# Optimization experiments

Hardware: AMD Instinct MI355X
Metric: run time of the kernel (lower is better)

## Reference

```python
import jax, jax.numpy as jnp
import numpy as np

B, C, H, W = 8, 256, 64, 64
CK = C // 8  # query/key channels


def setup_inputs() -> dict:
    key = jax.random.key(0)
    ks = jax.random.split(key, 8)
    s = 1.0 / np.sqrt(C)
    return {
        "x": jax.random.normal(ks[0], (B, C, H, W), dtype=jnp.float32),
        "Wq": jax.random.normal(ks[1], (CK, C), dtype=jnp.float32) * s,
        "bq": jax.random.normal(ks[2], (CK,), dtype=jnp.float32) * 0.01,
        "Wk": jax.random.normal(ks[3], (CK, C), dtype=jnp.float32) * s,
        "bk": jax.random.normal(ks[4], (CK,), dtype=jnp.float32) * 0.01,
        "Wv": jax.random.normal(ks[5], (C, C), dtype=jnp.float32) * s,
        "bv": jax.random.normal(ks[6], (C,), dtype=jnp.float32) * 0.01,
        "gamma": jax.random.normal(ks[7], (1,), dtype=jnp.float32) * 0.1,
    }


def reference(x, Wq, bq, Wk, bk, Wv, bv, gamma):
    b, c, h, w = x.shape
    n = h * w
    xf = x.reshape(b, c, n)                       # [B,C,N]
    # 1x1 convs == channel-wise linear maps
    q = jnp.einsum('oc,bcn->bon', Wq, xf) + bq[:, None]   # [B,CK,N]
    k = jnp.einsum('oc,bcn->bon', Wk, xf) + bk[:, None]   # [B,CK,N]
    v = jnp.einsum('oc,bcn->bon', Wv, xf) + bv[:, None]   # [B,C,N]
    energy = jnp.einsum('bcm,bcn->bmn', q, k)             # [B,N,N] (query rows m)
    attn = jax.nn.softmax(energy, axis=-1)
    out = jnp.einsum('bcn,bmn->bcm', v, attn)             # value @ attn^T
    out = out.reshape(b, c, h, w)
    return gamma * out + x
```

## Files before the change

kernel.cpp:

```cpp
#include <hip/hip_runtime.h>
#include <stdint.h>

typedef unsigned short u16;
typedef unsigned int u32;
typedef __bf16 bf16_t;
typedef __bf16 bf16x4 __attribute__((ext_vector_type(4)));
typedef __bf16 bf16x8 __attribute__((ext_vector_type(8)));
typedef float f32x4 __attribute__((ext_vector_type(4)));
typedef float f32x16 __attribute__((ext_vector_type(16)));

#define LOG2E 1.4426950408889634f
#define MFMA32(a, b, c) __builtin_amdgcn_mfma_f32_32x32x16_bf16(a, b, c, 0, 0, 0)

__device__ __forceinline__ u16 f2bf(float f) {
    union { float f; unsigned int u; } v; v.f = f;
    unsigned int r = v.u + 0x7fffu + ((v.u >> 16) & 1u);
    return (u16)(r >> 16);
}

__device__ __forceinline__ bf16x8 ld8f_bf(const float* __restrict__ p) {
    float4 a = *reinterpret_cast<const float4*>(p);
    float4 b = *reinterpret_cast<const float4*>(p + 4);
    bf16x8 r;
    r[0] = (bf16_t)a.x; r[1] = (bf16_t)a.y; r[2] = (bf16_t)a.z; r[3] = (bf16_t)a.w;
    r[4] = (bf16_t)b.x; r[5] = (bf16_t)b.y; r[6] = (bf16_t)b.z; r[7] = (bf16_t)b.w;
    return r;
}

__device__ __forceinline__ u32 cvt_pk_bf16(float a, float b) {
    u32 r;
    asm("v_cvt_pk_bf16_f32 %0, %1, %2" : "=v"(r) : "v"(a), "v"(b));
    return r;
}

__device__ __forceinline__ void plane32_swap(u32& a, u32& b) {
    asm("v_permlane32_swap_b32 %0, %1" : "+v"(a), "+v"(b));
}

__device__ __forceinline__ bf16x8 pack8(const float* p) {
    u32 c0 = cvt_pk_bf16(p[0], p[1]);
    u32 c1 = cvt_pk_bf16(p[2], p[3]);
    u32 c2 = cvt_pk_bf16(p[4], p[5]);
    u32 c3 = cvt_pk_bf16(p[6], p[7]);
    plane32_swap(c0, c2);
    plane32_swap(c1, c3);
    union { u32 u[4]; bf16x8 v; } f;
    f.u[0] = c0; f.u[1] = c1; f.u[2] = c2; f.u[3] = c3;
    return f.v;
}

__device__ __forceinline__ void g2lds16(const u16* g, u16* l) {
    __builtin_amdgcn_global_load_lds(
        (const __attribute__((address_space(1))) unsigned int*)g,
        (__attribute__((address_space(3))) unsigned int*)l, 16, 0, 0);
}

__global__ __launch_bounds__(256) void k_transpose(
    const float* __restrict__ x,
    const float* __restrict__ Wq, const float* __restrict__ Wk,
    const float* __restrict__ Wv,
    u16* __restrict__ xT, u16* __restrict__ wqkb, u16* __restrict__ wvb) {
    int blk = blockIdx.x;
    int t = threadIdx.x;
    if (blk >= 2048) {
        if (blk == 2048) {
            for (int j = 0; j < 8; ++j) {
                int fg = j * 256 + t;
                int n = fg >> 5, g = fg & 31;
                const float* src = (n < 32) ? (Wq + (size_t)n * 256 + g * 8)
                                            : (Wk + (size_t)(n - 32) * 256 + g * 8);
                *reinterpret_cast<bf16x8*>(wqkb + n * 256 + ((g ^ (n & 7)) << 3)) =
                    ld8f_bf(src);
            }
        } else {
            int base = (blk - 2049) * 2048;
            for (int j = 0; j < 8; ++j) {
                int fg = base + j * 256 + t;
                int slice = fg >> 10, d = fg & 1023;
                int co = d >> 2, g2 = (d & 3) ^ (co & 3);
                *reinterpret_cast<bf16x8*>(wvb + fg * 8) =
                    ld8f_bf(Wv + (size_t)co * 256 + slice * 32 + g2 * 8);
            }
        }
        return;
    }
    __shared__ u16 tile[64][68];
    int b = blk >> 8;
    int r = blk & 255;
    int c0 = (r & 3) * 64;
    int n0 = (r >> 2) * 64;
    const float* xb = x + (size_t)b * 256 * 4096;
    u16* xTb = xT + (size_t)b * 4096 * 256;
    int lc = t >> 4;
    int l4 = (t & 15) * 4;
    #pragma unroll
    for (int p = 0; p < 4; ++p) {
        int c = lc + p * 16;
        float4 v = *reinterpret_cast<const float4*>(xb + (size_t)(c0 + c) * 4096 + n0 + l4);
        tile[c][l4 + 0] = f2bf(v.x); tile[c][l4 + 1] = f2bf(v.y);
        tile[c][l4 + 2] = f2bf(v.z); tile[c][l4 + 3] = f2bf(v.w);
    }
    __syncthreads();
    #pragma unroll
    for (int p = 0; p < 4; ++p) {
        int n = lc + p * 16;
        ushort4 v;
        v.x = tile[l4 + 0][n]; v.y = tile[l4 + 1][n];
        v.z = tile[l4 + 2][n]; v.w = tile[l4 + 3][n];
        int gslot = ((c0 + l4) >> 3) ^ ((n0 + n) & 7);
        *reinterpret_cast<ushort4*>(
            xTb + (size_t)(n0 + n) * 256 + (gslot << 3) + (l4 & 7)) = v;
    }
}

__global__ __launch_bounds__(256, 2) void k_proj(
    const u16* __restrict__ xT, const u16* __restrict__ wqkb,
    const u16* __restrict__ wvb,
    const float* __restrict__ bq, const float* __restrict__ bk,
    const float* __restrict__ bv,
    u16* __restrict__ qt, u16* __restrict__ kt, u16* __restrict__ vt) {
    __shared__ u16 Xs[64 * 256];
    __shared__ u16 Ws[64 * 256];
    __shared__ u16 Wvs[256 * 32];
    int blk = blockIdx.x;
    int b = blk & 7;
    int n0 = (blk >> 3) * 64;
    int t = threadIdx.x;
    int w = t >> 6;
    int lane = t & 63;
    int lo = lane & 15;
    int q = lane >> 4;
    const u16* xTb = xT + (size_t)b * 4096 * 256;

    #pragma unroll
    for (int p = 0; p < 8; ++p) {
        g2lds16(xTb + (size_t)n0 * 256 + (p * 256 + t) * 8, &Xs[(p * 256 + w * 64) * 8]);
        g2lds16(wqkb + (p * 256 + t) * 8, &Ws[(p * 256 + w * 64) * 8]);
    }

    f32x4 accqk[4] = {};
    f32x4 accv[16];
    #pragma unroll
    for (int i = 0; i < 16; ++i) accv[i] = f32x4{0.f, 0.f, 0.f, 0.f};

    int rowA = w * 16 + lo;
    int cw = w * 64;
    for (int c0 = 0; c0 < 256; c0 += 32) {
        __syncthreads();
        #pragma unroll
        for (int p = 0; p < 4; ++p) {
            g2lds16(wvb + (size_t)(c0 >> 5) * 8192 + (p * 256 + t) * 8,
                    &Wvs[(p * 256 + w * 64) * 8]);
        }
        __syncthreads();

        int K = c0 >> 3;
        bf16x8 a = *reinterpret_cast<const bf16x8*>(
            &Xs[(rowA * 32 + ((K + q) ^ (lo & 7))) * 8]);
        #pragma unroll
        for (int ot = 0; ot < 4; ++ot) {
            bf16x8 bb = *reinterpret_cast<const bf16x8*>(
                &Ws[((ot * 16 + lo) * 32 + ((K + q) ^ (lo & 7))) * 8]);
            accqk[ot] = __builtin_amdgcn_mfma_f32_16x16x32_bf16(a, bb, accqk[ot], 0, 0, 0);
        }
        bf16x8 xbf[4];
        #pragma unroll
        for (int nt = 0; nt < 4; ++nt)
            xbf[nt] = *reinterpret_cast<const bf16x8*>(
                &Xs[((nt * 16 + lo) * 32 + ((K + q) ^ (lo & 7))) * 8]);
        #pragma unroll
        for (int ct = 0; ct < 4; ++ct) {
            int co = cw + ct * 16 + lo;
            bf16x8 av = *reinterpret_cast<const bf16x8*>(
                &Wvs[(co * 4 + (q ^ (co & 3))) * 8]);
            #pragma unroll
            for (int nt = 0; nt < 4; ++nt)
                accv[ct * 4 + nt] = __builtin_amdgcn_mfma_f32_16x16x32_bf16(
                    av, xbf[nt], accv[ct * 4 + nt], 0, 0, 0);
        }
    }
    #pragma unroll
    for (int ot = 0; ot < 4; ++ot) {
        float bias = (ot < 2) ? bq[ot * 16 + lo] : bk[(ot - 2) * 16 + lo];
        #pragma unroll
        for (int r = 0; r < 4; ++r) {
            int n = n0 + w * 16 + q * 4 + r;
            float val = accqk[ot][r] + bias;
            if (ot < 2) qt[((size_t)b * 4096 + n) * 32 + ot * 16 + lo] = f2bf(val * LOG2E);
            else        kt[((size_t)b * 4096 + n) * 32 + (ot - 2) * 16 + lo] = f2bf(val);
        }
    }
    #pragma unroll
    for (int ct = 0; ct < 4; ++ct) {
        #pragma unroll
        for (int nt = 0; nt < 4; ++nt) {
            int nt_g = (n0 >> 4) + nt;
            #pragma unroll
            for (int r = 0; r < 4; ++r) {
                int co = cw + ct * 16 + q * 4 + r;
                float val = accv[ct * 4 + nt][r] + bv[co];
                vt[(((size_t)b * 256 + nt_g) * 256 + co) * 16 + lo] = f2bf(val);
            }
        }
    }
}

#define FLASH_PV_HALF1(FC0, FC1, Vc_)                                          \
    {                                                                          \
        bf16x8 v0_ = *reinterpret_cast<const bf16x8*>(Vc_ + gslot8);           \
        bf16x8 v1_ = *reinterpret_cast<const bf16x8*>(Vc_ + 512 + gslot8);     \
        bf16x8 v2_ = *reinterpret_cast<const bf16x8*>(Vc_ + 1024 + gslot8);    \
        bf16x8 v3_ = *reinterpret_cast<const bf16x8*>(Vc_ + 1536 + gslot8);    \
        O0 = MFMA32(v0_, FC0, O0); O1 = MFMA32(v1_, FC0, O1);                  \
        O2 = MFMA32(v2_, FC0, O2); O3 = MFMA32(v3_, FC0, O3);                  \
        bf16x8 v4_ = *reinterpret_cast<const bf16x8*>(Vc_ + 2048 + gslot8);    \
        bf16x8 v5_ = *reinterpret_cast<const bf16x8*>(Vc_ + 2560 + gslot8);    \
        bf16x8 v6_ = *reinterpret_cast<const bf16x8*>(Vc_ + 3072 + gslot8);    \
        bf16x8 v7_ = *reinterpret_cast<const bf16x8*>(Vc_ + 3584 + gslot8);    \
        O0 = MFMA32(v4_, FC1, O0); O1 = MFMA32(v5_, FC1, O1);                  \
        O2 = MFMA32(v6_, FC1, O2); O3 = MFMA32(v7_, FC1, O3);                  \
    }

#define FLASH_PV_HALF2(FC2, FC3, Vc_)                                          \
    {                                                                          \
        bf16x8 v0_ = *reinterpret_cast<const bf16x8*>(Vc_ + 4096 + gslot8);    \
        bf16x8 v1_ = *reinterpret_cast<const bf16x8*>(Vc_ + 4608 + gslot8);    \
        bf16x8 v2_ = *reinterpret_cast<const bf16x8*>(Vc_ + 5120 + gslot8);    \
        bf16x8 v3_ = *reinterpret_cast<const bf16x8*>(Vc_ + 5632 + gslot8);    \
        O0 = MFMA32(v0_, FC2, O0); O1 = MFMA32(v1_, FC2, O1);                  \
        O2 = MFMA32(v2_, FC2, O2); O3 = MFMA32(v3_, FC2, O3);                  \
        bf16x8 v4_ = *reinterpret_cast<const bf16x8*>(Vc_ + 6144 + gslot8);    \
        bf16x8 v5_ = *reinterpret_cast<const bf16x8*>(Vc_ + 6656 + gslot8);    \
        bf16x8 v6_ = *reinterpret_cast<const bf16x8*>(Vc_ + 7168 + gslot8);    \
        bf16x8 v7_ = *reinterpret_cast<const bf16x8*>(Vc_ + 7680 + gslot8);    \
        O0 = MFMA32(v4_, FC3, O0); O1 = MFMA32(v5_, FC3, O1);                  \
        O2 = MFMA32(v6_, FC3, O2); O3 = MFMA32(v7_, FC3, O3);                  \
    }

#define FLASH_ITER(S_, KC0, KC1, KC2, KC3, KN0, KN1, KN2, KN3,                 \
                   FC0, FC1, FC2, FC3, FN0, FN1, FN2, FN3, VDN)                \
    {                                                                          \
        const int s_ = (S_);                                                   \
        const u16* kp_ = kbase + (size_t)(((s_ + 2) & 63) * 2048);             \
        KN0 = *reinterpret_cast<const bf16x8*>(kp_);                           \
        KN1 = *reinterpret_cast<const bf16x8*>(kp_ + 16);                      \
        KN2 = *reinterpret_cast<const bf16x8*>(kp_ + 1024);                    \
        KN3 = *reinterpret_cast<const bf16x8*>(kp_ + 1040);                    \
        const u16* vs_ = vstage + (size_t)(s_ + 1) * 16384;                    \
        g2lds16(vs_,        VDN);                                              \
        g2lds16(vs_ + 512,  VDN + 512);                                        \
        g2lds16(vs_ + 1024, VDN + 1024);                                       \
        g2lds16(vs_ + 1536, VDN + 1536);                                       \
        f32x16 S0_ = MFMA32(KC0, qf0, z16); S0_ = MFMA32(KC1, qf1, S0_);       \
        f32x16 S1_ = MFMA32(KC2, qf0, z16); S1_ = MFMA32(KC3, qf1, S1_);       \
        const u16* Vc_ = Vs[s_ & 1];                                           \
        float p0_[16];                                                         \
        _Pragma("unroll")                                                      \
        for (int i_ = 0; i_ < 16; ++i_) {                                      \
            p0_[i_] = __builtin_amdgcn_exp2f(S0_[i_]); lsum += p0_[i_];        \
        }                                                                      \
        FN0 = pack8(p0_); FN1 = pack8(p0_ + 8);                                \
        FLASH_PV_HALF1(FC0, FC1, Vc_)                                          \
        float p1_[16];                                                         \
        _Pragma("unroll")                                                      \
        for (int i_ = 0; i_ < 16; ++i_) {                                      \
            p1_[i_] = __builtin_amdgcn_exp2f(S1_[i_]); lsum += p1_[i_];        \
        }                                                                      \
        FN2 = pack8(p1_); FN3 = pack8(p1_ + 8);                                \
        FLASH_PV_HALF2(FC2, FC3, Vc_)                                          \
        __syncthreads();                                                       \
    }

__global__ __launch_bounds__(256, 2) void k_flash(
    const u16* __restrict__ qt, const u16* __restrict__ kt,
    const u16* __restrict__ vt, const float* __restrict__ x,
    const float* __restrict__ gamma, float* __restrict__ out) {
    __shared__ u16 Vs[2][8192];
    int blk = blockIdx.x;
    int b = blk & 7;
    int rest = blk >> 3;
    int m0 = (rest & 31) * 128;
    int ch0 = (rest >> 5) * 128;
    int t = threadIdx.x;
    int w = t >> 6;
    int lane = t & 63;
    int la = lane & 31;
    int hi = lane >> 5;

    const u16* qtb = qt + (size_t)b * 4096 * 32;
    const u16* ktb = kt + (size_t)b * 4096 * 32;
    const u16* vtb = vt + (size_t)b * 256 * 256 * 16;

    int qw0 = m0 + w * 32;
    bf16x8 qf0 = *reinterpret_cast<const bf16x8*>(qtb + (size_t)(qw0 + la) * 32 + hi * 8);
    bf16x8 qf1 = *reinterpret_cast<const bf16x8*>(qtb + (size_t)(qw0 + la) * 32 + 16 + hi * 8);

    const u16* kbase = ktb + (size_t)la * 32 + hi * 8;

    int g = la * 2 + hi;
    int gslot8 = (g ^ (g >> 3)) * 8;
    int sg = lane ^ (lane >> 3);
    const u16* vstage = vtb + ((size_t)(w * 256) + ch0) * 16 + sg * 8;
    u16* vd0 = &Vs[0][w * 2048];
    u16* vd1 = &Vs[1][w * 2048];

    f32x16 O0 = {}, O1 = {}, O2 = {}, O3 = {};
    const f32x16 z16 = {};
    float lsum = 0.f;

    bf16x8 kA0, kA1, kA2, kA3, kB0, kB1, kB2, kB3;
    bf16x8 fA0, fA1, fA2, fA3, fB0, fB1, fB2, fB3;

    kA0 = *reinterpret_cast<const bf16x8*>(kbase);
    kA1 = *reinterpret_cast<const bf16x8*>(kbase + 16);
    kA2 = *reinterpret_cast<const bf16x8*>(kbase + 1024);
    kA3 = *reinterpret_cast<const bf16x8*>(kbase + 1040);
    g2lds16(vstage,        vd0);
    g2lds16(vstage + 512,  vd0 + 512);
    g2lds16(vstage + 1024, vd0 + 1024);
    g2lds16(vstage + 1536, vd0 + 1536);
    kB0 = *reinterpret_cast<const bf16x8*>(kbase + 2048);
    kB1 = *reinterpret_cast<const bf16x8*>(kbase + 2064);
    kB2 = *reinterpret_cast<const bf16x8*>(kbase + 3072);
    kB3 = *reinterpret_cast<const bf16x8*>(kbase + 3088);
    {
        f32x16 S0 = MFMA32(kA0, qf0, z16); S0 = MFMA32(kA1, qf1, S0);
        f32x16 S1 = MFMA32(kA2, qf0, z16); S1 = MFMA32(kA3, qf1, S1);
        float p0[16], p1[16];
        #pragma unroll
        for (int i = 0; i < 16; ++i) { p0[i] = __builtin_amdgcn_exp2f(S0[i]); lsum += p0[i]; }
        fA0 = pack8(p0); fA1 = pack8(p0 + 8);
        #pragma unroll
        for (int i = 0; i < 16; ++i) { p1[i] = __builtin_amdgcn_exp2f(S1[i]); lsum += p1[i]; }
        fA2 = pack8(p1); fA3 = pack8(p1 + 8);
    }
    __syncthreads();

    for (int ss = 0; ss < 31; ++ss) {
        int s0 = ss * 2;
        FLASH_ITER(s0,     kB0, kB1, kB2, kB3, kA0, kA1, kA2, kA3,
                           fA0, fA1, fA2, fA3, fB0, fB1, fB2, fB3, vd1)
        FLASH_ITER(s0 + 1, kA0, kA1, kA2, kA3, kB0, kB1, kB2, kB3,
                           fB0, fB1, fB2, fB3, fA0, fA1, fA2, fA3, vd0)
    }
    FLASH_ITER(62, kB0, kB1, kB2, kB3, kA0, kA1, kA2, kA3,
                   fA0, fA1, fA2, fA3, fB0, fB1, fB2, fB3, vd1)
    {
        const u16* Vc_ = Vs[1];
        FLASH_PV_HALF1(fB0, fB1, Vc_)
        FLASH_PV_HALF2(fB2, fB3, Vc_)
    }

    lsum += __shfl_xor(lsum, 32, 64);
    float linv = 1.0f / lsum;
    float gm = gamma[0];
    const float* xb = x + (size_t)b * 256 * 4096;
    float* ob = out + (size_t)b * 256 * 4096;
    int m = m0 + w * 32 + la;
    #pragma unroll
    for (int r = 0; r < 16; ++r) {
        int crow = (r & 3) + 8 * (r >> 2) + 4 * hi;
        size_t i0 = (size_t)(ch0 + crow) * 4096 + m;
        ob[i0]             = gm * (O0[r] * linv) + xb[i0];
        ob[i0 + 32 * 4096] = gm * (O1[r] * linv) + xb[i0 + 32 * 4096];
        ob[i0 + 64 * 4096] = gm * (O2[r] * linv) + xb[i0 + 64 * 4096];
        ob[i0 + 96 * 4096] = gm * (O3[r] * linv) + xb[i0 + 96 * 4096];
    }
}

extern "C" void kernel_launch(void* const* d_in, const int* in_sizes, int n_in,
                              void* d_out, int out_size, void* d_ws, size_t ws_size,
                              hipStream_t stream) {
    const float* x     = (const float*)d_in[0];
    const float* Wq    = (const float*)d_in[1];
    const float* bq    = (const float*)d_in[2];
    const float* Wk    = (const float*)d_in[3];
    const float* bk    = (const float*)d_in[4];
    const float* Wv    = (const float*)d_in[5];
    const float* bv    = (const float*)d_in[6];
    const float* gamma = (const float*)d_in[7];
    float* out = (float*)d_out;

    char* ws = (char*)d_ws;
    u16* xT   = (u16*)d_out;
    u16* wqkb = (u16*)d_out + 8388608;
    u16* wvb  = (u16*)d_out + 8388608 + 16384;
    u16* qt = (u16*)ws;
    u16* kt = (u16*)(ws + 2097152);
    u16* vt = (u16*)(ws + 2 * 2097152);

    k_transpose<<<2053, 256, 0, stream>>>(x, Wq, Wk, Wv, xT, wqkb, wvb);
    k_proj<<<512, 256, 0, stream>>>(xT, wqkb, wvb, bq, bk, bv, qt, kt, vt);
    k_flash<<<512, 256, 0, stream>>>(qt, kt, vt, x, gamma, out);
}
```

Baseline: 199.9 us.

## Compute softmax row sums via MFMA, add setprio, read projection weights from global

The flash kernel now accumulates the softmax denominator with extra MFMAs against a vector of ones on the bf16-packed probabilities, replacing the scalar adds and the final cross-lane shuffle. This moves VALU work onto the matrix unit but sums rounded bf16 values. s_setprio is raised around the PV MFMA groups to favour matrix issue across waves. The projection kernel drops its LDS staging of the Wqk and Wv weights and their per-iteration barriers, loading weights straight from global or cache instead and fully unrolling the channel loop.

```diff
diff --git a/kernel.cpp b/kernel.cpp
--- a/kernel.cpp
+++ b/kernel.cpp
@@ -120,8 +120,6 @@
     const float* __restrict__ bv,
     u16* __restrict__ qt, u16* __restrict__ kt, u16* __restrict__ vt) {
     __shared__ u16 Xs[64 * 256];
-    __shared__ u16 Ws[64 * 256];
-    __shared__ u16 Wvs[256 * 32];
     int blk = blockIdx.x;
     int b = blk & 7;
     int n0 = (blk >> 3) * 64;
@@ -133,10 +131,8 @@
     const u16* xTb = xT + (size_t)b * 4096 * 256;
 
     #pragma unroll
-    for (int p = 0; p < 8; ++p) {
+    for (int p = 0; p < 8; ++p)
         g2lds16(xTb + (size_t)n0 * 256 + (p * 256 + t) * 8, &Xs[(p * 256 + w * 64) * 8]);
-        g2lds16(wqkb + (p * 256 + t) * 8, &Ws[(p * 256 + w * 64) * 8]);
-    }
 
     f32x4 accqk[4] = {};
     f32x4 accv[16];
@@ -145,22 +141,17 @@
 
     int rowA = w * 16 + lo;
     int cw = w * 64;
+    __syncthreads();
+
+    #pragma unroll
     for (int c0 = 0; c0 < 256; c0 += 32) {
-        __syncthreads();
-        #pragma unroll
-        for (int p = 0; p < 4; ++p) {
-            g2lds16(wvb + (size_t)(c0 >> 5) * 8192 + (p * 256 + t) * 8,
-                    &Wvs[(p * 256 + w * 64) * 8]);
-        }
-        __syncthreads();
-
         int K = c0 >> 3;
         bf16x8 a = *reinterpret_cast<const bf16x8*>(
             &Xs[(rowA * 32 + ((K + q) ^ (lo & 7))) * 8]);
         #pragma unroll
         for (int ot = 0; ot < 4; ++ot) {
             bf16x8 bb = *reinterpret_cast<const bf16x8*>(
-                &Ws[((ot * 16 + lo) * 32 + ((K + q) ^ (lo & 7))) * 8]);
+                wqkb + ((ot * 16 + lo) * 32 + ((K + q) ^ (lo & 7))) * 8);
             accqk[ot] = __builtin_amdgcn_mfma_f32_16x16x32_bf16(a, bb, accqk[ot], 0, 0, 0);
         }
         bf16x8 xbf[4];
@@ -172,7 +163,7 @@
         for (int ct = 0; ct < 4; ++ct) {
             int co = cw + ct * 16 + lo;
             bf16x8 av = *reinterpret_cast<const bf16x8*>(
-                &Wvs[(co * 4 + (q ^ (co & 3))) * 8]);
+                wvb + (size_t)(c0 >> 5) * 8192 + (co * 4 + (q ^ (co & 3))) * 8);
             #pragma unroll
             for (int nt = 0; nt < 4; ++nt)
                 accv[ct * 4 + nt] = __builtin_amdgcn_mfma_f32_16x16x32_bf16(
@@ -211,14 +202,18 @@
         bf16x8 v1_ = *reinterpret_cast<const bf16x8*>(Vc_ + 512 + gslot8);     \
         bf16x8 v2_ = *reinterpret_cast<const bf16x8*>(Vc_ + 1024 + gslot8);    \
         bf16x8 v3_ = *reinterpret_cast<const bf16x8*>(Vc_ + 1536 + gslot8);    \
+        __builtin_amdgcn_s_setprio(1);                                         \
         O0 = MFMA32(v0_, FC0, O0); O1 = MFMA32(v1_, FC0, O1);                  \
         O2 = MFMA32(v2_, FC0, O2); O3 = MFMA32(v3_, FC0, O3);                  \
+        __builtin_amdgcn_s_setprio(0);                                         \
         bf16x8 v4_ = *reinterpret_cast<const bf16x8*>(Vc_ + 2048 + gslot8);    \
         bf16x8 v5_ = *reinterpret_cast<const bf16x8*>(Vc_ + 2560 + gslot8);    \
         bf16x8 v6_ = *reinterpret_cast<const bf16x8*>(Vc_ + 3072 + gslot8);    \
         bf16x8 v7_ = *reinterpret_cast<const bf16x8*>(Vc_ + 3584 + gslot8);    \
+        __builtin_amdgcn_s_setprio(1);                                         \
         O0 = MFMA32(v4_, FC1, O0); O1 = MFMA32(v5_, FC1, O1);                  \
         O2 = MFMA32(v6_, FC1, O2); O3 = MFMA32(v7_, FC1, O3);                  \
+        __builtin_amdgcn_s_setprio(0);                                         \
     }
 
 #define FLASH_PV_HALF2(FC2, FC3, Vc_)                                          \
@@ -227,14 +222,18 @@
         bf16x8 v1_ = *reinterpret_cast<const bf16x8*>(Vc_ + 4608 + gslot8);    \
         bf16x8 v2_ = *reinterpret_cast<const bf16x8*>(Vc_ + 5120 + gslot8);    \
         bf16x8 v3_ = *reinterpret_cast<const bf16x8*>(Vc_ + 5632 + gslot8);    \
+        __builtin_amdgcn_s_setprio(1);                                         \
         O0 = MFMA32(v0_, FC2, O0); O1 = MFMA32(v1_, FC2, O1);                  \
         O2 = MFMA32(v2_, FC2, O2); O3 = MFMA32(v3_, FC2, O3);                  \
+        __builtin_amdgcn_s_setprio(0);                                         \
         bf16x8 v4_ = *reinterpret_cast<const bf16x8*>(Vc_ + 6144 + gslot8);    \
         bf16x8 v5_ = *reinterpret_cast<const bf16x8*>(Vc_ + 6656 + gslot8);    \
         bf16x8 v6_ = *reinterpret_cast<const bf16x8*>(Vc_ + 7168 + gslot8);    \
         bf16x8 v7_ = *reinterpret_cast<const bf16x8*>(Vc_ + 7680 + gslot8);    \
+        __builtin_amdgcn_s_setprio(1);                                         \
         O0 = MFMA32(v4_, FC3, O0); O1 = MFMA32(v5_, FC3, O1);                  \
         O2 = MFMA32(v6_, FC3, O2); O3 = MFMA32(v7_, FC3, O3);                  \
+        __builtin_amdgcn_s_setprio(0);                                         \
     }
 
 #define FLASH_ITER(S_, KC0, KC1, KC2, KC3, KN0, KN1, KN2, KN3,                 \
@@ -256,17 +255,15 @@
         const u16* Vc_ = Vs[s_ & 1];                                           \
         float p0_[16];                                                         \
         _Pragma("unroll")                                                      \
-        for (int i_ = 0; i_ < 16; ++i_) {                                      \
-            p0_[i_] = __builtin_amdgcn_exp2f(S0_[i_]); lsum += p0_[i_];        \
-        }                                                                      \
+        for (int i_ = 0; i_ < 16; ++i_) p0_[i_] = __builtin_amdgcn_exp2f(S0_[i_]); \
         FN0 = pack8(p0_); FN1 = pack8(p0_ + 8);                                \
+        Lacc = MFMA32(ones, FN0, Lacc); Lacc = MFMA32(ones, FN1, Lacc);        \
         FLASH_PV_HALF1(FC0, FC1, Vc_)                                          \
         float p1_[16];                                                         \
         _Pragma("unroll")                                                      \
-        for (int i_ = 0; i_ < 16; ++i_) {                                      \
-            p1_[i_] = __builtin_amdgcn_exp2f(S1_[i_]); lsum += p1_[i_];        \
-        }                                                                      \
+        for (int i_ = 0; i_ < 16; ++i_) p1_[i_] = __builtin_amdgcn_exp2f(S1_[i_]); \
         FN2 = pack8(p1_); FN3 = pack8(p1_ + 8);                                \
+        Lacc = MFMA32(ones, FN2, Lacc); Lacc = MFMA32(ones, FN3, Lacc);        \
         FLASH_PV_HALF2(FC2, FC3, Vc_)                                          \
         __syncthreads();                                                       \
     }
@@ -305,8 +302,11 @@
     u16* vd1 = &Vs[1][w * 2048];
 
     f32x16 O0 = {}, O1 = {}, O2 = {}, O3 = {};
+    f32x16 Lacc = {};
     const f32x16 z16 = {};
-    float lsum = 0.f;
+    bf16x8 ones;
+    #pragma unroll
+    for (int i = 0; i < 8; ++i) ones[i] = (bf16_t)1.0f;
 
     bf16x8 kA0, kA1, kA2, kA3, kB0, kB1, kB2, kB3;
     bf16x8 fA0, fA1, fA2, fA3, fB0, fB1, fB2, fB3;
@@ -328,11 +328,13 @@
         f32x16 S1 = MFMA32(kA2, qf0, z16); S1 = MFMA32(kA3, qf1, S1);
         float p0[16], p1[16];
         #pragma unroll
-        for (int i = 0; i < 16; ++i) { p0[i] = __builtin_amdgcn_exp2f(S0[i]); lsum += p0[i]; }
+        for (int i = 0; i < 16; ++i) p0[i] = __builtin_amdgcn_exp2f(S0[i]);
         fA0 = pack8(p0); fA1 = pack8(p0 + 8);
         #pragma unroll
-        for (int i = 0; i < 16; ++i) { p1[i] = __builtin_amdgcn_exp2f(S1[i]); lsum += p1[i]; }
+        for (int i = 0; i < 16; ++i) p1[i] = __builtin_amdgcn_exp2f(S1[i]);
         fA2 = pack8(p1); fA3 = pack8(p1 + 8);
+        Lacc = MFMA32(ones, fA0, Lacc); Lacc = MFMA32(ones, fA1, Lacc);
+        Lacc = MFMA32(ones, fA2, Lacc); Lacc = MFMA32(ones, fA3, Lacc);
     }
     __syncthreads();
 
@@ -351,8 +353,7 @@
         FLASH_PV_HALF2(fB2, fB3, Vc_)
     }
 
-    lsum += __shfl_xor(lsum, 32, 64);
-    float linv = 1.0f / lsum;
+    float linv = 1.0f / Lacc[0];
     float gm = gamma[0];
     const float* xb = x + (size_t)b * 256 * 4096;
     float* ob = out + (size_t)b * 256 * 4096;
```

After: 210.0 us. 5.0% more time.
